# Optimization experiments

Measured on AMD Instinct MI355X. Metric: run time of the kernel, lower is better.

The kernel has to match this reference:

```python
import jax, jax.numpy as jnp
import numpy as np

N = 200000          # graph_size (stalk rows)
H = 128             # hidden_channels
NNZ = 3200000       # Laplacian nnz (avg degree 16)
K = 15              # polynomial degree (poly_layers_K)
LAMBDA_MAX = 2.0    # normalised Laplacian -> analytic lambda_max


def setup_inputs() -> dict:
    key = jax.random.key(0)
    ks = jax.random.split(key, 6)
    x = jax.random.normal(ks[0], (N, H), dtype=jnp.float32)
    vals = jax.random.normal(ks[1], (NNZ,), dtype=jnp.float32)
    poly_logits = jax.random.normal(ks[2], (K + 1,), dtype=jnp.float32)
    hp_alpha = jax.random.normal(ks[3], (), dtype=jnp.float32)
    edge_row = jax.random.randint(ks[4], (NNZ,), 0, N, dtype=jnp.int64)
    edge_col = jax.random.randint(ks[5], (NNZ,), 0, N, dtype=jnp.int64)
    return {"x": x, "vals": vals, "poly_logits": poly_logits,
            "hp_alpha": hp_alpha, "edge_row": edge_row, "edge_col": edge_col}


def reference(x, vals, poly_logits, hp_alpha, edge_row, edge_col):
    n = x.shape[0]

    def spmm(v):  # (n,h) -> (n,h), sparse L @ v in COO form
        return jax.ops.segment_sum(vals[:, None] * v[edge_col], edge_row,
                                   num_segments=n)

    def Lhat(v):  # L_hat = (2/lambda_max) L - I
        return (2.0 / LAMBDA_MAX) * spmm(v) - v

    w = jax.nn.softmax(poly_logits)  # mixture over Chebyshev T_0..T_K

    # Chebyshev Type-1 recurrence: T_{k+1} = 2 L_hat T_k - T_{k-1}
    T0 = x
    T1 = Lhat(x)
    out = w[0] * T0 + w[1] * T1

    def step(carry, wk):
        T0, T1, out = carry
        Tk1 = 2.0 * Lhat(T1) - T0
        return (T1, Tk1, out + wk * Tk1), None

    (_, _, px), _ = jax.lax.scan(step, (T0, T1, out), w[2:])

    # high-pass term: x - (1/lambda_max) L x
    hp = x - spmm(x) / LAMBDA_MAX
    return -px + hp_alpha * hp
```

## Files before the change

### kernel.cpp

```cpp
#include <hip/hip_runtime.h>
#include <math.h>

#define N_NODES 200000
#define H_CH    128
#define GRP     64
#define NNZ_E   3200000
#define K_DEG   15

__global__ void softmax_k(const float* __restrict__ logits, float* __restrict__ w) {
    if (threadIdx.x == 0) {
        float m = -1e30f;
        for (int i = 0; i <= K_DEG; ++i) m = fmaxf(m, logits[i]);
        float e[K_DEG + 1];
        float s = 0.f;
        for (int i = 0; i <= K_DEG; ++i) { e[i] = expf(logits[i] - m); s += e[i]; }
        float inv = 1.0f / s;
        for (int i = 0; i <= K_DEG; ++i) w[i] = e[i] * inv;
    }
}

__global__ void hist_k(const int* __restrict__ row, int* __restrict__ counts, int nnz) {
    int i = blockIdx.x * blockDim.x + threadIdx.x;
    if (i < nnz) atomicAdd(&counts[row[i]], 1);
}

__global__ void scan1_k(const int* __restrict__ counts, int* __restrict__ out,
                        int* __restrict__ partials, int n) {
    __shared__ int sm[256];
    int tbase = blockIdx.x * 2048 + threadIdx.x * 8;
    int v[8];
    int tsum = 0;
#pragma unroll
    for (int j = 0; j < 8; ++j) {
        int i = tbase + j;
        int c = (i < n) ? counts[i] : 0;
        v[j] = tsum;
        tsum += c;
    }
    sm[threadIdx.x] = tsum;
    __syncthreads();
    int incl = tsum;
    for (int off = 1; off < 256; off <<= 1) {
        int t = (threadIdx.x >= (unsigned)off) ? sm[threadIdx.x - off] : 0;
        __syncthreads();
        incl += t;
        sm[threadIdx.x] = incl;
        __syncthreads();
    }
    int texcl = incl - tsum;
    if (threadIdx.x == 255) partials[blockIdx.x] = incl;
#pragma unroll
    for (int j = 0; j < 8; ++j) {
        int i = tbase + j;
        if (i < n) out[i] = texcl + v[j];
    }
}

__global__ void scan2_k(int* partials, int nb, int* row_ptr, int n, int total) {
    __shared__ int sm[128];
    int v = (threadIdx.x < (unsigned)nb) ? partials[threadIdx.x] : 0;
    sm[threadIdx.x] = v;
    __syncthreads();
    int incl = v;
    for (int off = 1; off < 128; off <<= 1) {
        int t = (threadIdx.x >= (unsigned)off) ? sm[threadIdx.x - off] : 0;
        __syncthreads();
        incl += t;
        sm[threadIdx.x] = incl;
        __syncthreads();
    }
    if (threadIdx.x < (unsigned)nb) partials[threadIdx.x] = incl - v;
    if (threadIdx.x == 0) row_ptr[n] = total;
}

__global__ void scan3_k(int* __restrict__ row_ptr, const int* __restrict__ partials,
                        int* __restrict__ fill, int n) {
    int off = partials[blockIdx.x];
    int tbase = blockIdx.x * 2048 + threadIdx.x * 8;
#pragma unroll
    for (int j = 0; j < 8; ++j) {
        int i = tbase + j;
        if (i < n) {
            int v = row_ptr[i] + off;
            row_ptr[i] = v;
            fill[i] = v;
        }
    }
}

__global__ void scatter_k(const int* __restrict__ row, const int* __restrict__ col,
                          const float* __restrict__ vals, int* __restrict__ fill,
                          int2* __restrict__ csr, int nnz) {
    int i = blockIdx.x * blockDim.x + threadIdx.x;
    if (i < nnz) {
        int r = row[i];
        int p = atomicAdd(&fill[r], 1);
        int2 cv;
        cv.x = col[i];
        cv.y = __float_as_int(vals[i]);
        csr[p] = cv;
    }
}

__global__ __launch_bounds__(256) void first_k(
    const int* __restrict__ rp, const int2* __restrict__ csr,
    const float* __restrict__ x, float* __restrict__ T1g, float* __restrict__ out,
    const float* __restrict__ w, const float* __restrict__ alpha_p, int goff) {
    int wid = blockIdx.x * 4 + (threadIdx.x >> 6);
    int r = __builtin_amdgcn_readfirstlane(wid);
    if (r >= N_NODES) return;
    int lane = threadIdx.x & 63;
    const float* base = x + goff + lane;
    int e0 = rp[r], e1 = rp[r + 1];
    float a0 = 0.f, a1 = 0.f, a2 = 0.f, a3 = 0.f;
    int e = e0;
    for (; e + 4 <= e1; e += 4) {
        int2 cv0 = csr[e], cv1 = csr[e + 1], cv2 = csr[e + 2], cv3 = csr[e + 3];
        a0 = fmaf(__int_as_float(cv0.y), base[(size_t)cv0.x * H_CH], a0);
        a1 = fmaf(__int_as_float(cv1.y), base[(size_t)cv1.x * H_CH], a1);
        a2 = fmaf(__int_as_float(cv2.y), base[(size_t)cv2.x * H_CH], a2);
        a3 = fmaf(__int_as_float(cv3.y), base[(size_t)cv3.x * H_CH], a3);
    }
    for (; e < e1; ++e) {
        int2 cv = csr[e];
        a0 = fmaf(__int_as_float(cv.y), base[(size_t)cv.x * H_CH], a0);
    }
    float s = (a0 + a1) + (a2 + a3);
    size_t idxg = (size_t)r * GRP + lane;
    size_t idxf = (size_t)r * H_CH + goff + lane;
    float xr = x[idxf];
    float w0 = w[0], w1 = w[1], al = alpha_p[0];
    float t1 = s - xr;
    float o = -(w0 * xr + w1 * t1) + al * (xr - 0.5f * s);
    T1g[idxg] = t1;
    out[idxf] = o;
}

__global__ __launch_bounds__(256) void cheb_k(
    const int* __restrict__ rp, const int2* __restrict__ csr,
    const float* __restrict__ Tcur, const float* TprevBase, int tprevStride,
    float* Tnext, float* __restrict__ out,
    const float* __restrict__ w, int k, int goff) {
    int wid = blockIdx.x * 4 + (threadIdx.x >> 6);
    int r = __builtin_amdgcn_readfirstlane(wid);
    if (r >= N_NODES) return;
    int lane = threadIdx.x & 63;
    const float* base = Tcur + lane;
    int e0 = rp[r], e1 = rp[r + 1];
    float a0 = 0.f, a1 = 0.f, a2 = 0.f, a3 = 0.f;
    int e = e0;
    for (; e + 4 <= e1; e += 4) {
        int2 cv0 = csr[e], cv1 = csr[e + 1], cv2 = csr[e + 2], cv3 = csr[e + 3];
        a0 = fmaf(__int_as_float(cv0.y), base[(size_t)cv0.x * GRP], a0);
        a1 = fmaf(__int_as_float(cv1.y), base[(size_t)cv1.x * GRP], a1);
        a2 = fmaf(__int_as_float(cv2.y), base[(size_t)cv2.x * GRP], a2);
        a3 = fmaf(__int_as_float(cv3.y), base[(size_t)cv3.x * GRP], a3);
    }
    for (; e < e1; ++e) {
        int2 cv = csr[e];
        a0 = fmaf(__int_as_float(cv.y), base[(size_t)cv.x * GRP], a0);
    }
    float s = (a0 + a1) + (a2 + a3);
    size_t idxg = (size_t)r * GRP + lane;
    size_t idxf = (size_t)r * H_CH + goff + lane;
    float tc = Tcur[idxg];
    float tp = TprevBase[(size_t)r * tprevStride + lane];
    float wk = w[k];
    float tn = 2.0f * (s - tc) - tp;
    float o = out[idxf];
    o -= wk * tn;
    out[idxf] = o;
    Tnext[idxg] = tn;
}

extern "C" void kernel_launch(void* const* d_in, const int* in_sizes, int n_in,
                              void* d_out, int out_size, void* d_ws, size_t ws_size,
                              hipStream_t stream) {
    const float* x      = (const float*)d_in[0];
    const float* vals   = (const float*)d_in[1];
    const float* logits = (const float*)d_in[2];
    const float* alpha  = (const float*)d_in[3];
    const int*   erow   = (const int*)d_in[4];
    const int*   ecol   = (const int*)d_in[5];
    float* out = (float*)d_out;

    const size_t NG = (size_t)N_NODES * GRP;
    float* bufA    = (float*)d_ws;
    float* bufB    = bufA + NG;
    int2*  csr     = (int2*)(bufB + NG);
    int*   row_ptr = (int*)(csr + NNZ_E);
    int*   counts  = row_ptr + (N_NODES + 1);
    int*   fill    = counts + N_NODES;
    int*   partials= fill + N_NODES;
    float* w_buf   = (float*)(partials + 128);

    hipMemsetAsync(counts, 0, N_NODES * sizeof(int), stream);
    softmax_k<<<1, 64, 0, stream>>>(logits, w_buf);
    hist_k<<<(NNZ_E + 255) / 256, 256, 0, stream>>>(erow, counts, NNZ_E);

    const int TILE = 2048;
    int nblk = (N_NODES + TILE - 1) / TILE;
    scan1_k<<<nblk, 256, 0, stream>>>(counts, row_ptr, partials, N_NODES);
    scan2_k<<<1, 128, 0, stream>>>(partials, nblk, row_ptr, N_NODES, NNZ_E);
    scan3_k<<<nblk, 256, 0, stream>>>(row_ptr, partials, fill, N_NODES);
    scatter_k<<<(NNZ_E + 255) / 256, 256, 0, stream>>>(erow, ecol, vals, fill, csr, NNZ_E);

    int grid = (N_NODES + 3) / 4;

    for (int g = 0; g < H_CH / GRP; ++g) {
        int goff = g * GRP;
        first_k<<<grid, 256, 0, stream>>>(row_ptr, csr, x, bufB, out, w_buf, alpha, goff);
        cheb_k<<<grid, 256, 0, stream>>>(row_ptr, csr, bufB, x + goff, H_CH, bufA,
                                         out, w_buf, 2, goff);
        float* Tcur = bufA;
        float* Tprev = bufB;
        for (int k = 3; k <= K_DEG; ++k) {
            cheb_k<<<grid, 256, 0, stream>>>(row_ptr, csr, Tcur, Tprev, GRP, Tprev,
                                             out, w_buf, k, goff);
            float* t = Tcur; Tcur = Tprev; Tprev = t;
        }
    }
}
```

Before: 4.695 ms.

## Replace random COO-to-CSR scatter with two-pass bucketed staging, add nontemporal hints

COO-to-CSR construction now runs in two passes. The first pass groups edges into 512-row buckets in shared memory and writes them contiguously to a staging buffer. The second pass scatters each bucket into CSR, so atomics and writes stay within a small row window. This replaces fully random global atomics and stores. The Chebyshev kernels also use nontemporal loads and stores for the output and previous-term streams to reduce cache pollution. Costs are a large staging workspace, a fixed bucket capacity (BCAP) that could overflow on skewed row distributions, and extra shared-memory use that limits occupancy.

```diff
diff --git a/kernel.cpp b/kernel.cpp
--- a/kernel.cpp
+++ b/kernel.cpp
@@ -6,6 +6,11 @@
 #define GRP     64
 #define NNZ_E   3200000
 #define K_DEG   15
+
+#define EPB     4096
+#define BSHIFT  9
+#define NBUCK   391
+#define BCAP    9216
 
 __global__ void softmax_k(const float* __restrict__ logits, float* __restrict__ w) {
     if (threadIdx.x == 0) {
@@ -19,9 +24,85 @@
     }
 }
 
-__global__ void hist_k(const int* __restrict__ row, int* __restrict__ counts, int nnz) {
-    int i = blockIdx.x * blockDim.x + threadIdx.x;
-    if (i < nnz) atomicAdd(&counts[row[i]], 1);
+__global__ __launch_bounds__(256) void bucketA_k(
+    const int* __restrict__ row, const int* __restrict__ col,
+    const float* __restrict__ vals, int* __restrict__ counts,
+    int* __restrict__ gfill, uint2* __restrict__ stag, int nnz) {
+    __shared__ int cnt[NBUCK];
+    __shared__ int excl[NBUCK];
+    __shared__ int gbase[NBUCK];
+    __shared__ int sm[256];
+    __shared__ uint2 sstag[EPB];
+    __shared__ unsigned short sb[EPB];
+
+    int tid = threadIdx.x;
+    int base = blockIdx.x * EPB;
+
+    for (int t = tid; t < NBUCK; t += 256) cnt[t] = 0;
+    __syncthreads();
+
+    int r[16], c[16], b[16];
+    float v[16];
+#pragma unroll
+    for (int j = 0; j < 16; ++j) {
+        int i = base + j * 256 + tid;
+        if (i < nnz) {
+            r[j] = row[i]; c[j] = col[i]; v[j] = vals[i];
+            b[j] = r[j] >> BSHIFT;
+            atomicAdd(&cnt[b[j]], 1);
+            atomicAdd(&counts[r[j]], 1);
+        } else {
+            b[j] = -1;
+        }
+    }
+    __syncthreads();
+
+    {
+        int b0 = 2 * tid, b1 = 2 * tid + 1;
+        int c0 = (b0 < NBUCK) ? cnt[b0] : 0;
+        int c1 = (b1 < NBUCK) ? cnt[b1] : 0;
+        int pair = c0 + c1;
+        sm[tid] = pair;
+        __syncthreads();
+        int incl = pair;
+        for (int off = 1; off < 256; off <<= 1) {
+            int tv = (tid >= off) ? sm[tid - off] : 0;
+            __syncthreads();
+            incl += tv;
+            sm[tid] = incl;
+            __syncthreads();
+        }
+        int pexcl = incl - pair;
+        if (b0 < NBUCK) excl[b0] = pexcl;
+        if (b1 < NBUCK) excl[b1] = pexcl + c0;
+    }
+    __syncthreads();
+
+    for (int t = tid; t < NBUCK; t += 256) {
+        int cb = cnt[t];
+        gbase[t] = (cb > 0) ? atomicAdd(&gfill[t], cb) : 0;
+    }
+    __syncthreads();
+    for (int t = tid; t < NBUCK; t += 256) cnt[t] = excl[t];
+    __syncthreads();
+
+#pragma unroll
+    for (int j = 0; j < 16; ++j) {
+        if (b[j] >= 0) {
+            int p = atomicAdd(&cnt[b[j]], 1);
+            sstag[p] = make_uint2(((unsigned)(r[j] & 511) << 18) | (unsigned)c[j],
+                                  __float_as_uint(v[j]));
+            sb[p] = (unsigned short)b[j];
+        }
+    }
+    __syncthreads();
+
+    int tot = nnz - base; if (tot > EPB) tot = EPB;
+    for (int i = tid; i < tot; i += 256) {
+        int bb = sb[i];
+        size_t gp = (size_t)bb * BCAP + gbase[bb] + (i - excl[bb]);
+        stag[gp] = sstag[i];
+    }
 }
 
 __global__ void scan1_k(const int* __restrict__ counts, int* __restrict__ out,
@@ -88,16 +169,21 @@
     }
 }
 
-__global__ void scatter_k(const int* __restrict__ row, const int* __restrict__ col,
-                          const float* __restrict__ vals, int* __restrict__ fill,
-                          int2* __restrict__ csr, int nnz) {
-    int i = blockIdx.x * blockDim.x + threadIdx.x;
-    if (i < nnz) {
-        int r = row[i];
-        int p = atomicAdd(&fill[r], 1);
+__global__ __launch_bounds__(256) void bucketB_k(
+    const uint2* __restrict__ stag, const int* __restrict__ gfill,
+    int* __restrict__ fill, int2* __restrict__ csr) {
+    int b = blockIdx.x;
+    int n = gfill[b];
+    const uint2* s = stag + (size_t)b * BCAP;
+    for (int i = threadIdx.x; i < n; i += 256) {
+        uint2 e = s[i];
+        int rl = (int)(e.x >> 18);
+        int cc = (int)(e.x & 0x3FFFF);
+        int rr = (b << BSHIFT) | rl;
+        int p = atomicAdd(&fill[rr], 1);
         int2 cv;
-        cv.x = col[i];
-        cv.y = __float_as_int(vals[i]);
+        cv.x = cc;
+        cv.y = (int)e.y;
         csr[p] = cv;
     }
 }
@@ -133,7 +219,7 @@
     float t1 = s - xr;
     float o = -(w0 * xr + w1 * t1) + al * (xr - 0.5f * s);
     T1g[idxg] = t1;
-    out[idxf] = o;
+    __builtin_nontemporal_store(o, &out[idxf]);
 }
 
 __global__ __launch_bounds__(256) void cheb_k(
@@ -164,12 +250,12 @@
     size_t idxg = (size_t)r * GRP + lane;
     size_t idxf = (size_t)r * H_CH + goff + lane;
     float tc = Tcur[idxg];
-    float tp = TprevBase[(size_t)r * tprevStride + lane];
+    float tp = __builtin_nontemporal_load(&TprevBase[(size_t)r * tprevStride + lane]);
     float wk = w[k];
     float tn = 2.0f * (s - tc) - tp;
-    float o = out[idxf];
+    float o = __builtin_nontemporal_load(&out[idxf]);
     o -= wk * tn;
-    out[idxf] = o;
+    __builtin_nontemporal_store(o, &out[idxf]);
     Tnext[idxg] = tn;
 }
 
@@ -188,22 +274,26 @@
     float* bufA    = (float*)d_ws;
     float* bufB    = bufA + NG;
     int2*  csr     = (int2*)(bufB + NG);
-    int*   row_ptr = (int*)(csr + NNZ_E);
+    uint2* stag    = (uint2*)(csr + NNZ_E);
+    int*   row_ptr = (int*)(stag + (size_t)NBUCK * BCAP);
     int*   counts  = row_ptr + (N_NODES + 1);
-    int*   fill    = counts + N_NODES;
+    int*   gfill   = counts + N_NODES;
+    int*   fill    = gfill + NBUCK;
     int*   partials= fill + N_NODES;
     float* w_buf   = (float*)(partials + 128);
 
-    hipMemsetAsync(counts, 0, N_NODES * sizeof(int), stream);
+    hipMemsetAsync(counts, 0, (N_NODES + NBUCK) * sizeof(int), stream);
     softmax_k<<<1, 64, 0, stream>>>(logits, w_buf);
-    hist_k<<<(NNZ_E + 255) / 256, 256, 0, stream>>>(erow, counts, NNZ_E);
+
+    int nblkA = (NNZ_E + EPB - 1) / EPB;
+    bucketA_k<<<nblkA, 256, 0, stream>>>(erow, ecol, vals, counts, gfill, stag, NNZ_E);
 
     const int TILE = 2048;
     int nblk = (N_NODES + TILE - 1) / TILE;
     scan1_k<<<nblk, 256, 0, stream>>>(counts, row_ptr, partials, N_NODES);
     scan2_k<<<1, 128, 0, stream>>>(partials, nblk, row_ptr, N_NODES, NNZ_E);
     scan3_k<<<nblk, 256, 0, stream>>>(row_ptr, partials, fill, N_NODES);
-    scatter_k<<<(NNZ_E + 255) / 256, 256, 0, stream>>>(erow, ecol, vals, fill, csr, NNZ_E);
+    bucketB_k<<<NBUCK, 256, 0, stream>>>(stag, gfill, fill, csr);
 
     int grid = (N_NODES + 3) / 4;
 
```

New measurement: 4.618 ms. No clear change (-1.6%).
